# Kernel tuning notes

Measured on AMD Instinct MI355X. Metric: run time of the kernel, lower is better.

The kernel has to match this reference:

```python
import jax, jax.numpy as jnp
import numpy as np

N_CRYST = 64
ATOMS_PER = 32
N = N_CRYST * ATOMS_PER          # 2048 atoms
NBR = 20                         # max_neighbors
E = N * NBR                      # 40960 edges
C = 128                          # sphere_channels(_reduce)
HID = 256                        # hidden_channels
NB = 128                         # num_basis_functions
NLAYER = 8                       # num_interactions
LMAX = 6
K = 1 + 3 * LMAX                 # SH coeffs with mmax=1 -> 19
MAXZ = 100                       # MAX_ATOMIC_NUM
ZDIM = 256
CUT = 8.0
FOUR_PI = 4.0 * np.pi


def sph_harm_m01(d):
    """Real spherical harmonics Y_l^m, l<=LMAX, m in {-1,0,1}. d: [E,3] unit vecs -> [E,K]."""
    x, y, ct = d[:, 0], d[:, 1], d[:, 2]
    rho = jnp.sqrt(x * x + y * y) + 1e-12   # sin(theta)
    cph, sph = x / rho, y / rho
    # Legendre P_l(ct)
    P0 = [jnp.ones_like(ct), ct]
    for l in range(2, LMAX + 1):
        P0.append(((2 * l - 1) * ct * P0[l - 1] - (l - 1) * P0[l - 2]) / l)
    # Associated Legendre P_l^1(ct)
    P1 = {1: -rho, 2: -3.0 * ct * rho}
    for l in range(3, LMAX + 1):
        P1[l] = ((2 * l - 1) * ct * P1[l - 1] - l * P1[l - 2]) / (l - 1)
    Ys = [jnp.full_like(ct, float(np.sqrt(1.0 / FOUR_PI)))]
    for l in range(1, LMAX + 1):
        K0 = float(np.sqrt((2 * l + 1) / FOUR_PI))
        K1 = float(np.sqrt(2.0 * (2 * l + 1) / FOUR_PI / (l * (l + 1))))
        Ys += [K1 * P1[l] * sph, K0 * P0[l], K1 * P1[l] * cph]  # m=-1,0,+1
    return jnp.stack(Ys, axis=-1)


def lattice_from_params(lengths, angles):
    """lengths,angles(deg): [B,3] -> lattice row-vectors [B,3,3]."""
    a, b, c = lengths[:, 0], lengths[:, 1], lengths[:, 2]
    rad = angles * (np.pi / 180.0)
    ca, cb, cg = jnp.cos(rad[:, 0]), jnp.cos(rad[:, 1]), jnp.cos(rad[:, 2])
    sg = jnp.sin(rad[:, 2])
    z0 = jnp.zeros_like(a)
    v3y = (ca - cb * cg) / sg
    v3z = jnp.sqrt(jnp.clip(1.0 - cb * cb - v3y * v3y, 1e-8))
    l1 = jnp.stack([a, z0, z0], -1)
    l2 = jnp.stack([b * cg, b * sg, z0], -1)
    l3 = jnp.stack([c * cb, c * v3y, c * v3z], -1)
    return jnp.stack([l1, l2, l3], axis=1)


def setup_inputs() -> dict:
    key = jax.random.key(0)
    ks = jax.random.split(key, 16)
    z = jax.random.normal(ks[0], (N_CRYST, ZDIM), jnp.float32)
    frac = jax.random.uniform(ks[1], (N, 3), jnp.float32)
    atom_types = jax.random.randint(ks[2], (N,), 1, MAXZ + 1)
    num_atoms = jnp.full((N_CRYST,), ATOMS_PER, jnp.int32)
    lengths = 4.0 + 4.0 * jax.random.uniform(ks[3], (N_CRYST, 3), jnp.float32)
    angles = 80.0 + 20.0 * jax.random.uniform(ks[4], (N_CRYST, 3), jnp.float32)
    batch = jnp.arange(N) // ATOMS_PER
    # NBR incoming edges per atom, sources restricted to the same crystal
    dst = jnp.repeat(jnp.arange(N), NBR)
    src_local = jax.random.randint(ks[5], (E,), 0, ATOMS_PER)
    src = (dst // ATOMS_PER) * ATOMS_PER + src_local
    edge_index = jnp.stack([src, dst], axis=0)
    sc = lambda k, sh, fan: jax.random.normal(k, sh, jnp.float32) / np.sqrt(fan)
    params = dict(
        emb=sc(ks[6], (MAXZ + 1, C), 1.0),
        zproj=sc(ks[7], (ZDIM, C), ZDIM),
        Wd=sc(ks[8], (NLAYER, NB, HID), NB),
        W1=sc(ks[9], (NLAYER, C, HID), C),
        W2=sc(ks[10], (NLAYER, HID, C), HID),
        Wa=sc(ks[11], (C, MAXZ), C),
        ba=jnp.zeros((MAXZ,), jnp.float32),
        wf=sc(ks[12], (C,), C),
    )
    return dict(z=z, pred_frac_coords=frac, pred_atom_types=atom_types,
                num_atoms=num_atoms, lengths=lengths, angles=angles,
                batch=batch, edge_index=edge_index, **params)


def reference(z, pred_frac_coords, pred_atom_types, num_atoms, lengths, angles,
              batch, edge_index, emb, zproj, Wd, W1, W2, Wa, ba, wf):
    lat = lattice_from_params(lengths, angles)                 # [B,3,3]
    pos = jnp.einsum('ni,nij->nj', pred_frac_coords, lat[batch])  # [N,3]
    src, dst = edge_index[0], edge_index[1]
    vec = pos[src] - pos[dst]                                  # [E,3]
    dist = jnp.linalg.norm(vec, axis=-1) + 1e-8
    dirn = vec / dist[:, None]
    offsets = jnp.linspace(0.0, CUT, NB)
    width = offsets[1] - offsets[0]
    rbf = jnp.exp(-0.5 * ((dist[:, None] - offsets) / width) ** 2)  # [E,NB]
    Y = sph_harm_m01(dirn)                                     # [E,K]
    # node SH features, l=0 initialized from atom embedding + latent
    x = jnp.zeros((N, K, C), pred_frac_coords.dtype)
    x = x.at[:, 0, :].set(emb[pred_atom_types] + (z @ zproj)[batch])
    for l in range(NLAYER):
        s = jnp.einsum('ek,ekc->ec', Y, x[src])                # project along edge frame
        h = jax.nn.silu(s @ W1[l] + rbf @ Wd[l])               # [E,HID]
        m = h @ W2[l]                                          # [E,C]
        agg = jax.ops.segment_sum(Y[:, :, None] * m[:, None, :], dst, num_segments=N)
        x = x + agg / NBR
    h_node = x[:, 0, :]                                        # [N,C]
    atom_logits = h_node @ Wa + ba                             # [N,MAXZ]
    fscal = (h_node[src] - h_node[dst]) @ wf                   # [E]
    coord_diff = jax.ops.segment_sum(fscal[:, None] * dirn, dst, num_segments=N)
    return coord_diff, atom_logits
```

## Files before the change

kernel.cpp:

```cpp
#include <hip/hip_runtime.h>
#include <hip/hip_bf16.h>

#define N_CRYST 64
#define ATOMS_PER 32
#define NN 2048
#define NBRS 20
#define EE 40960
#define CC 128
#define HIDDIM 256
#define NBASIS 128
#define NLAYERS 8
#define LMAXV 6
#define KK 19
#define MAXZV 100
#define ZDIMV 256
#define FOUR_PI_F 12.566370614359172f

typedef unsigned short ushort_t;
typedef __attribute__((ext_vector_type(8))) short short8;
typedef __attribute__((ext_vector_type(4))) float floatx4;

__device__ __forceinline__ ushort_t f2us(float f) {
    union { float f; unsigned u; } x;
    x.f = f;
    unsigned r = (x.u + 0x7fffu + ((x.u >> 16) & 1u)) >> 16;
    return (ushort_t)r;
}
__device__ __forceinline__ float us2f(unsigned u) {
    return __uint_as_float(u << 16);
}

__global__ void k_pos(const float* __restrict__ frac, const float* __restrict__ lengths,
                      const float* __restrict__ angles, const int* __restrict__ batch,
                      float* __restrict__ pos) {
    int n = blockIdx.x * blockDim.x + threadIdx.x;
    if (n >= NN) return;
    int b = batch[n];
    float la = lengths[b * 3 + 0];
    float lb = lengths[b * 3 + 1];
    float lc = lengths[b * 3 + 2];
    const float D2R = 0.017453292519943295f;
    float aa = angles[b * 3 + 0] * D2R;
    float ab = angles[b * 3 + 1] * D2R;
    float ag = angles[b * 3 + 2] * D2R;
    float ca = cosf(aa), cb = cosf(ab), cg = cosf(ag), sg = sinf(ag);
    float v3y = (ca - cb * cg) / sg;
    float v3z = sqrtf(fmaxf(1.0f - cb * cb - v3y * v3y, 1e-8f));
    float f0 = frac[n * 3 + 0];
    float f1 = frac[n * 3 + 1];
    float f2 = frac[n * 3 + 2];
    pos[n * 3 + 0] = f0 * la + f1 * (lb * cg) + f2 * (lc * cb);
    pos[n * 3 + 1] = f1 * (lb * sg) + f2 * (lc * v3y);
    pos[n * 3 + 2] = f2 * (lc * v3z);
}

__global__ void k_edge(const int* __restrict__ ei, const float* __restrict__ pos,
                       float* __restrict__ dist, float* __restrict__ dirn,
                       float* __restrict__ Yv) {
    int e = blockIdx.x * blockDim.x + threadIdx.x;
    if (e >= EE) return;
    int s = ei[e], d = ei[EE + e];
    float vx = pos[s * 3 + 0] - pos[d * 3 + 0];
    float vy = pos[s * 3 + 1] - pos[d * 3 + 1];
    float vz = pos[s * 3 + 2] - pos[d * 3 + 2];
    float dd = sqrtf(vx * vx + vy * vy + vz * vz) + 1e-8f;
    float ix = vx / dd, iy = vy / dd, iz = vz / dd;
    dist[e] = dd;
    dirn[e * 3 + 0] = ix;
    dirn[e * 3 + 1] = iy;
    dirn[e * 3 + 2] = iz;

    float ct = iz;
    float rho = sqrtf(ix * ix + iy * iy) + 1e-12f;
    float cph = ix / rho, sph = iy / rho;
    float P0[LMAXV + 1];
    float P1[LMAXV + 1];
    P0[0] = 1.0f;
    P0[1] = ct;
    #pragma unroll
    for (int l = 2; l <= LMAXV; l++)
        P0[l] = ((2 * l - 1) * ct * P0[l - 1] - (l - 1) * P0[l - 2]) / (float)l;
    P1[0] = 0.0f;
    P1[1] = -rho;
    P1[2] = -3.0f * ct * rho;
    #pragma unroll
    for (int l = 3; l <= LMAXV; l++)
        P1[l] = ((2 * l - 1) * ct * P1[l - 1] - l * P1[l - 2]) / (float)(l - 1);

    float* Ye = Yv + (size_t)e * KK;
    Ye[0] = 0.28209479177387814f;
    #pragma unroll
    for (int l = 1; l <= LMAXV; l++) {
        float K0 = sqrtf((2 * l + 1) / FOUR_PI_F);
        float K1 = sqrtf(2.0f * (2 * l + 1) / (FOUR_PI_F * l * (l + 1)));
        Ye[3 * l - 2] = K1 * P1[l] * sph;
        Ye[3 * l - 1] = K0 * P0[l];
        Ye[3 * l]     = K1 * P1[l] * cph;
    }
}

__global__ void k_tcsr(const int* __restrict__ ei, int* __restrict__ trp,
                       int* __restrict__ tloc) {
    int bid = blockIdx.x;
    int t = threadIdx.x;
    __shared__ int cnt[32], base[32];
    if (t < 32) cnt[t] = 0;
    __syncthreads();
    int e0 = bid * 80;
    int abase = (bid >> 3) * 32;
    for (int j = t; j < 80; j += 64) {
        int a = ei[e0 + j] - abase;
        atomicAdd(&cnt[a], 1);
    }
    __syncthreads();
    if (t == 0) {
        int run = 0;
        for (int a = 0; a < 32; a++) {
            base[a] = run;
            trp[bid * 33 + a] = run;
            run += cnt[a];
        }
        trp[bid * 33 + 32] = run;
    }
    __syncthreads();
    if (t < 32) cnt[t] = 0;
    __syncthreads();
    for (int j = t; j < 80; j += 64) {
        int a = ei[e0 + j] - abase;
        int slot = base[a] + atomicAdd(&cnt[a], 1);
        tloc[bid * 80 + slot] = j;
    }
}

__global__ void k_rbfA(const float* __restrict__ dist, ushort_t* __restrict__ Abf) {
    int idx = blockIdx.x * blockDim.x + threadIdx.x;
    if (idx >= EE * NBASIS) return;
    int e = idx >> 7, j = idx & 127;
    const float width = 8.0f / 127.0f;
    const float invw = 127.0f / 8.0f;
    float t = (dist[e] - (float)j * width) * invw;
    Abf[(size_t)e * 256 + 128 + j] = f2us(expf(-0.5f * t * t));
}

__global__ void k_wt(const float* __restrict__ W1, const float* __restrict__ Wd,
                     const float* __restrict__ W2,
                     ushort_t* __restrict__ WT1, ushort_t* __restrict__ WT2) {
    int idx = blockIdx.x * blockDim.x + threadIdx.x;
    const int n1 = NLAYERS * HIDDIM * 256;
    if (idx < n1) {
        int l = idx >> 16;
        int r = idx & 65535;
        int n = r >> 8, k = r & 255;
        float v = (k < 128) ? W1[((size_t)l * CC + k) * HIDDIM + n]
                            : Wd[((size_t)l * NBASIS + (k - 128)) * HIDDIM + n];
        WT1[idx] = f2us(v);
    } else {
        int j = idx - n1;
        if (j >= NLAYERS * CC * HIDDIM) return;
        int l = j >> 15;
        int r = j & 32767;
        int n = r >> 8, k = r & 255;
        WT2[j] = f2us(W2[((size_t)l * HIDDIM + k) * CC + n]);
    }
}

__global__ void k_zc(const float* __restrict__ z, const float* __restrict__ zproj,
                     float* __restrict__ zc) {
    int idx = blockIdx.x * blockDim.x + threadIdx.x;
    if (idx >= N_CRYST * CC) return;
    int b = idx >> 7, c = idx & 127;
    float acc = 0.0f;
    for (int d = 0; d < ZDIMV; d++)
        acc += z[b * ZDIMV + d] * zproj[d * CC + c];
    zc[idx] = acc;
}

__global__ void k_xinit(const int* __restrict__ atype, const int* __restrict__ batch,
                        const float* __restrict__ emb, const float* __restrict__ zc,
                        float* __restrict__ x, ushort_t* __restrict__ xbf) {
    int idx = blockIdx.x * blockDim.x + threadIdx.x;
    if (idx >= NN * KK * CC) return;
    int n = idx / (KK * CC);
    int r = idx - n * (KK * CC);
    float v = 0.0f;
    if (r < CC) v = emb[atype[n] * CC + r] + zc[batch[n] * CC + r];
    x[idx] = v;
    xbf[idx] = f2us(v);
}

__global__ __launch_bounds__(512, 2) void k_layer(const int* __restrict__ trp,
                                                  const int* __restrict__ tloc,
                                                  const float* __restrict__ Yv,
                                                  const ushort_t* __restrict__ Abf,
                                                  const ushort_t* __restrict__ WT1,
                                                  const ushort_t* __restrict__ WT2,
                                                  const float* __restrict__ xin,
                                                  float* __restrict__ xout,
                                                  const ushort_t* __restrict__ xbfin,
                                                  ushort_t* __restrict__ xbfout) {
    __shared__ char smraw[47360];
    ushort_t* As  = (ushort_t*)smraw;
    ushort_t* Hs  = (ushort_t*)smraw;
    ushort_t* Ms  = (ushort_t*)smraw;
    float*   Ylds = (float*)(smraw + 40960);

    const int t = threadIdx.x;
    const int bid = blockIdx.x;
    const int w = t >> 6, lane = t & 63;
    const int quad = lane >> 4, lrow = lane & 15;
    const int e0 = bid * 80;
    const int cr = bid >> 3;

    const float* Yb = Yv + (size_t)e0 * KK;
    #pragma unroll
    for (int j = 0; j < 3; j++) {
        int i = t + j * 512;
        if (i < 80 * KK) Ylds[(i / KK) * 20 + (i % KK)] = Yb[i];
    }
    if (t < 80) Ylds[t * 20 + 19] = 0.f;
    __syncthreads();

    short8 arg[3];
    #pragma unroll
    for (int i = 0; i < 3; i++) {
        int idx = i * 512 + t;
        if (idx < 1280) {
            int r = idx >> 4, g16 = idx & 15;
            arg[i] = *(const short8*)(Abf + (size_t)(e0 + r) * 256 + 128 + g16 * 8);
        }
    }

    const int c2 = lane * 2;
    const int sgrp = lane >> 2;
    const int soff = (lane & 3) * 2;
    #pragma unroll 1
    for (int a8 = 0; a8 < 4; a8++) {
        const int a = w * 4 + a8;
        const int i0 = trp[bid * 33 + a];
        const int i1 = trp[bid * 33 + a + 1];
        if (i0 == i1) continue;
        const ushort_t* xsrc = xbfin + (size_t)(cr * 32 + a) * (KK * CC) + c2;
        float2 xr[KK];
        #pragma unroll
        for (int k = 0; k < KK; k++) {
            unsigned u = *(const unsigned*)(xsrc + k * CC);
            xr[k] = make_float2(us2f(u & 0xffffu), us2f(u >> 16));
        }
        for (int i = i0; i < i1; i++) {
            const int r = tloc[bid * 80 + i];
            const float* yp = Ylds + r * 20;
            float ax = 0.f, ay = 0.f;
            #pragma unroll
            for (int k = 0; k < KK; k++) {
                float y = yp[k];
                ax += y * xr[k].x;
                ay += y * xr[k].y;
            }
            unsigned pk = (unsigned)f2us(ax) | (((unsigned)f2us(ay)) << 16);
            *(unsigned*)&As[r * 256 + ((sgrp ^ (r & 7)) << 3) + soff] = pk;
        }
    }

    #pragma unroll
    for (int i = 0; i < 3; i++) {
        int idx = i * 512 + t;
        if (idx < 1280) {
            int r = idx >> 4, g = 16 + (idx & 15);
            *(short8*)&As[r * 256 + ((g ^ (r & 7)) << 3)] = arg[i];
        }
    }

    const ushort_t* W1w = WT1 + (size_t)(w * 32) * 256;
    short8 bp0[2], bp1[2];
    #pragma unroll
    for (int ni = 0; ni < 2; ni++) {
        bp0[ni] = *(const short8*)(W1w + (size_t)(ni * 16 + lrow) * 256 + quad * 8);
        bp1[ni] = *(const short8*)(W1w + (size_t)(ni * 16 + lrow) * 256 + 32 + quad * 8);
    }
    __syncthreads();

    floatx4 acc[5][2];
    #pragma unroll
    for (int mi = 0; mi < 5; mi++)
        #pragma unroll
        for (int ni = 0; ni < 2; ni++) acc[mi][ni] = (floatx4){0.f, 0.f, 0.f, 0.f};

    #pragma unroll
    for (int s8 = 0; s8 < 8; s8++) {
        short8 bcur[2];
        if (s8 & 1) {
            #pragma unroll
            for (int ni = 0; ni < 2; ni++) bcur[ni] = bp1[ni];
            if (s8 < 6) {
                const int kn = (s8 + 2) * 32 + quad * 8;
                #pragma unroll
                for (int ni = 0; ni < 2; ni++)
                    bp1[ni] = *(const short8*)(W1w + (size_t)(ni * 16 + lrow) * 256 + kn);
            }
        } else {
            #pragma unroll
            for (int ni = 0; ni < 2; ni++) bcur[ni] = bp0[ni];
            if (s8 < 6) {
                const int kn = (s8 + 2) * 32 + quad * 8;
                #pragma unroll
                for (int ni = 0; ni < 2; ni++)
                    bp0[ni] = *(const short8*)(W1w + (size_t)(ni * 16 + lrow) * 256 + kn);
            }
        }
        const int grp = s8 * 4 + quad;
        short8 af[5];
        #pragma unroll
        for (int mi = 0; mi < 5; mi++) {
            const int r = mi * 16 + lrow;
            af[mi] = *(const short8*)&As[r * 256 + ((grp ^ (r & 7)) << 3)];
        }
        #pragma unroll
        for (int ni = 0; ni < 2; ni++)
            #pragma unroll
            for (int mi = 0; mi < 5; mi++)
                acc[mi][ni] = __builtin_amdgcn_mfma_f32_16x16x32_bf16(
                    af[mi], bcur[ni], acc[mi][ni], 0, 0, 0);
    }

    const ushort_t* W2w = WT2 + (size_t)(w * 16) * 256;
    short8 bq0, bq1;
    bq0 = *(const short8*)(W2w + (size_t)lrow * 256 + quad * 8);
    bq1 = *(const short8*)(W2w + (size_t)lrow * 256 + 32 + quad * 8);
    __syncthreads();

    #pragma unroll
    for (int mi = 0; mi < 5; mi++) {
        const int row = mi * 16 + quad * 4;
        #pragma unroll
        for (int ni = 0; ni < 2; ni++) {
            const int col = w * 32 + ni * 16 + lrow;
            #pragma unroll
            for (int r = 0; r < 4; r++) {
                float v = acc[mi][ni][r];
                v = v * __builtin_amdgcn_rcpf(1.0f + __expf(-v));
                const int rr = row + r;
                Hs[rr * 256 + ((((col >> 3) ^ (rr & 7)) << 3) | (col & 7))] = f2us(v);
            }
        }
    }
    __syncthreads();

    floatx4 macc[5];
    #pragma unroll
    for (int mi = 0; mi < 5; mi++) macc[mi] = (floatx4){0.f, 0.f, 0.f, 0.f};

    #pragma unroll
    for (int s8 = 0; s8 < 8; s8++) {
        short8 bcur;
        if (s8 & 1) {
            bcur = bq1;
            if (s8 < 6) {
                const int kn = (s8 + 2) * 32 + quad * 8;
                bq1 = *(const short8*)(W2w + (size_t)lrow * 256 + kn);
            }
        } else {
            bcur = bq0;
            if (s8 < 6) {
                const int kn = (s8 + 2) * 32 + quad * 8;
                bq0 = *(const short8*)(W2w + (size_t)lrow * 256 + kn);
            }
        }
        const int grp = s8 * 4 + quad;
        short8 af[5];
        #pragma unroll
        for (int mi = 0; mi < 5; mi++) {
            const int r = mi * 16 + lrow;
            af[mi] = *(const short8*)&Hs[r * 256 + ((grp ^ (r & 7)) << 3)];
        }
        #pragma unroll
        for (int mi = 0; mi < 5; mi++)
            macc[mi] = __builtin_amdgcn_mfma_f32_16x16x32_bf16(
                af[mi], bcur, macc[mi], 0, 0, 0);
    }
    __syncthreads();

    #pragma unroll
    for (int mi = 0; mi < 5; mi++) {
        const int row = mi * 16 + quad * 4;
        const int col = w * 16 + lrow;
        #pragma unroll
        for (int r = 0; r < 4; r++)
            Ms[(row + r) * 132 + col] = f2us(macc[mi][r]);
    }
    __syncthreads();

    const int node = t >> 7;
    const int cq = t & 127;
    const int ng = bid * 4 + node;
    const float* xpi = xin + (size_t)ng * (KK * CC) + cq;
    float* xpo = xout + (size_t)ng * (KK * CC) + cq;
    ushort_t* xbp = xbfout + (size_t)ng * (KK * CC) + cq;

    float xold[KK];
    #pragma unroll
    for (int k = 0; k < KK; k++) xold[k] = xpi[k * CC];

    float xacc[KK];
    #pragma unroll
    for (int k = 0; k < KK; k++) xacc[k] = 0.f;

    #pragma unroll 4
    for (int e = 0; e < NBRS; e++) {
        const int eg = node * NBRS + e;
        const float m0 = us2f((unsigned)Ms[eg * 132 + cq]);
        const float* yp = Ylds + eg * 20;
        #pragma unroll
        for (int kq = 0; kq < 5; kq++) {
            float4 y = *(const float4*)(yp + kq * 4);
            const int k = kq * 4;
            xacc[k + 0] += y.x * m0;
            xacc[k + 1] += y.y * m0;
            xacc[k + 2] += y.z * m0;
            if (kq < 4) xacc[k + 3] += y.w * m0;
        }
    }
    const float s = 1.0f / (float)NBRS;
    #pragma unroll
    for (int k = 0; k < KK; k++) {
        float nv = xold[k] + xacc[k] * s;
        xpo[k * CC] = nv;
        xbp[k * CC] = f2us(nv);
    }
}

__global__ void k_logits(const float* __restrict__ x, const float* __restrict__ Wa,
                         const float* __restrict__ ba, float* __restrict__ out) {
    int idx = blockIdx.x * blockDim.x + threadIdx.x;
    if (idx >= NN * MAXZV) return;
    int n = idx / MAXZV, a = idx - n * MAXZV;
    float acc = ba[a];
    const float* hn = x + (size_t)n * (KK * CC);
    for (int c = 0; c < CC; c++) acc += hn[c] * Wa[c * MAXZV + a];
    out[idx] = acc;
}

__global__ void k_coord(const int* __restrict__ ei, const float* __restrict__ x,
                        const float* __restrict__ wf, const float* __restrict__ dirn,
                        float* __restrict__ out) {
    int n = blockIdx.x;
    int t = threadIdx.x;
    __shared__ float fs[NBRS];
    __shared__ float wsh[CC];
    wsh[t] = wf[t];
    wsh[t + 64] = wf[t + 64];
    __syncthreads();
    if (t < NBRS) {
        int e = n * NBRS + t;
        int sidx = ei[e];
        const float* xs = x + (size_t)sidx * (KK * CC);
        const float* xd = x + (size_t)n * (KK * CC);
        float acc = 0.0f;
        for (int c = 0; c < CC; c++) acc += (xs[c] - xd[c]) * wsh[c];
        fs[t] = acc;
    }
    __syncthreads();
    if (t < 3) {
        float acc = 0.0f;
        #pragma unroll
        for (int j = 0; j < NBRS; j++) acc += fs[j] * dirn[(size_t)(n * NBRS + j) * 3 + t];
        out[n * 3 + t] = acc;
    }
}

extern "C" void kernel_launch(void* const* d_in, const int* in_sizes, int n_in,
                              void* d_out, int out_size, void* d_ws, size_t ws_size,
                              hipStream_t stream) {
    (void)in_sizes; (void)n_in; (void)out_size; (void)ws_size;
    const float* z       = (const float*)d_in[0];
    const float* frac    = (const float*)d_in[1];
    const int*   atype   = (const int*)d_in[2];
    const float* lengths = (const float*)d_in[4];
    const float* angles  = (const float*)d_in[5];
    const int*   batch   = (const int*)d_in[6];
    const int*   ei      = (const int*)d_in[7];
    const float* emb     = (const float*)d_in[8];
    const float* zproj   = (const float*)d_in[9];
    const float* Wd      = (const float*)d_in[10];
    const float* W1      = (const float*)d_in[11];
    const float* W2      = (const float*)d_in[12];
    const float* Wa      = (const float*)d_in[13];
    const float* ba      = (const float*)d_in[14];
    const float* wf      = (const float*)d_in[15];
    float* out = (float*)d_out;

    float* ws = (float*)d_ws;
    float* pos  = ws; ws += NN * 3 + 4;
    float* dist = ws; ws += EE;
    float* dirn = ws; ws += EE * 3;
    float* Yv   = ws; ws += (size_t)EE * KK + 4;
    float* zc   = ws; ws += N_CRYST * CC;
    float* xA   = ws; ws += (size_t)NN * KK * CC;
    float* xB   = ws; ws += (size_t)NN * KK * CC;
    ushort_t* xbfA = (ushort_t*)ws; ws += (size_t)NN * KK * CC / 2;
    ushort_t* xbfB = (ushort_t*)ws; ws += (size_t)NN * KK * CC / 2;
    int* trp  = (int*)ws;
    int* tloc = trp + 512 * 33;
    ushort_t* Abf  = (ushort_t*)(tloc + 512 * 80);
    ushort_t* WT1  = Abf + (size_t)EE * 256;
    ushort_t* WT2  = WT1 + (size_t)NLAYERS * 256 * 256;

    k_pos<<<NN / 256, 256, 0, stream>>>(frac, lengths, angles, batch, pos);
    k_edge<<<EE / 256, 256, 0, stream>>>(ei, pos, dist, dirn, Yv);
    k_tcsr<<<512, 64, 0, stream>>>(ei, trp, tloc);
    k_rbfA<<<(EE * NBASIS) / 256, 256, 0, stream>>>(dist, Abf);
    k_wt<<<(NLAYERS * (HIDDIM * 256 + CC * HIDDIM)) / 256, 256, 0, stream>>>(W1, Wd, W2, WT1, WT2);
    k_zc<<<(N_CRYST * CC) / 256, 256, 0, stream>>>(z, zproj, zc);
    k_xinit<<<(NN * KK * CC) / 256, 256, 0, stream>>>(atype, batch, emb, zc, xA, xbfA);

    for (int l = 0; l < NLAYERS; l++) {
        const float* xi = (l & 1) ? xB : xA;
        float*       xo = (l & 1) ? xA : xB;
        const ushort_t* xbi = (l & 1) ? xbfB : xbfA;
        ushort_t*       xbo = (l & 1) ? xbfA : xbfB;
        k_layer<<<512, 512, 0, stream>>>(trp, tloc, Yv, Abf,
                                         WT1 + (size_t)l * 256 * 256,
                                         WT2 + (size_t)l * CC * HIDDIM,
                                         xi, xo, xbi, xbo);
    }

    k_coord<<<NN, 64, 0, stream>>>(ei, xA, wf, dirn, out);
    k_logits<<<(NN * MAXZV) / 256, 256, 0, stream>>>(xA, Wa, ba, out + NN * 3);
}
```

Measured before the change: 502.5 us.

## Fuse setup kernels, drop fp32 node state, merge output heads

Merges the position, edge geometry and CSR-building kernels into one per-crystal kernel that keeps positions in shared memory. Folds the latent projection into the node-init kernel and combines the coordinate and logits heads into a single launch. Removes the fp32 copy of the node features, so each layer now reads and writes only the bf16 state. This cuts launches and memory traffic, but the residual stream is now accumulated in bf16 across layers, which can hurt accuracy. The init kernel also recomputes the 256-long projection for every atom instead of once per crystal.

After: 480.4 us. 4.4% less time.

```diff
diff --git a/kernel.cpp b/kernel.cpp
--- a/kernel.cpp
+++ b/kernel.cpp
@@ -30,105 +30,99 @@
     return __uint_as_float(u << 16);
 }
 
-__global__ void k_pos(const float* __restrict__ frac, const float* __restrict__ lengths,
-                      const float* __restrict__ angles, const int* __restrict__ batch,
-                      float* __restrict__ pos) {
-    int n = blockIdx.x * blockDim.x + threadIdx.x;
-    if (n >= NN) return;
-    int b = batch[n];
-    float la = lengths[b * 3 + 0];
-    float lb = lengths[b * 3 + 1];
-    float lc = lengths[b * 3 + 2];
-    const float D2R = 0.017453292519943295f;
-    float aa = angles[b * 3 + 0] * D2R;
-    float ab = angles[b * 3 + 1] * D2R;
-    float ag = angles[b * 3 + 2] * D2R;
-    float ca = cosf(aa), cb = cosf(ab), cg = cosf(ag), sg = sinf(ag);
-    float v3y = (ca - cb * cg) / sg;
-    float v3z = sqrtf(fmaxf(1.0f - cb * cb - v3y * v3y, 1e-8f));
-    float f0 = frac[n * 3 + 0];
-    float f1 = frac[n * 3 + 1];
-    float f2 = frac[n * 3 + 2];
-    pos[n * 3 + 0] = f0 * la + f1 * (lb * cg) + f2 * (lc * cb);
-    pos[n * 3 + 1] = f1 * (lb * sg) + f2 * (lc * v3y);
-    pos[n * 3 + 2] = f2 * (lc * v3z);
-}
-
-__global__ void k_edge(const int* __restrict__ ei, const float* __restrict__ pos,
+__global__ void k_geom(const float* __restrict__ frac, const float* __restrict__ lengths,
+                       const float* __restrict__ angles, const int* __restrict__ ei,
                        float* __restrict__ dist, float* __restrict__ dirn,
-                       float* __restrict__ Yv) {
-    int e = blockIdx.x * blockDim.x + threadIdx.x;
-    if (e >= EE) return;
-    int s = ei[e], d = ei[EE + e];
-    float vx = pos[s * 3 + 0] - pos[d * 3 + 0];
-    float vy = pos[s * 3 + 1] - pos[d * 3 + 1];
-    float vz = pos[s * 3 + 2] - pos[d * 3 + 2];
-    float dd = sqrtf(vx * vx + vy * vy + vz * vz) + 1e-8f;
-    float ix = vx / dd, iy = vy / dd, iz = vz / dd;
-    dist[e] = dd;
-    dirn[e * 3 + 0] = ix;
-    dirn[e * 3 + 1] = iy;
-    dirn[e * 3 + 2] = iz;
-
-    float ct = iz;
-    float rho = sqrtf(ix * ix + iy * iy) + 1e-12f;
-    float cph = ix / rho, sph = iy / rho;
-    float P0[LMAXV + 1];
-    float P1[LMAXV + 1];
-    P0[0] = 1.0f;
-    P0[1] = ct;
-    #pragma unroll
-    for (int l = 2; l <= LMAXV; l++)
-        P0[l] = ((2 * l - 1) * ct * P0[l - 1] - (l - 1) * P0[l - 2]) / (float)l;
-    P1[0] = 0.0f;
-    P1[1] = -rho;
-    P1[2] = -3.0f * ct * rho;
-    #pragma unroll
-    for (int l = 3; l <= LMAXV; l++)
-        P1[l] = ((2 * l - 1) * ct * P1[l - 1] - l * P1[l - 2]) / (float)(l - 1);
-
-    float* Ye = Yv + (size_t)e * KK;
-    Ye[0] = 0.28209479177387814f;
-    #pragma unroll
-    for (int l = 1; l <= LMAXV; l++) {
-        float K0 = sqrtf((2 * l + 1) / FOUR_PI_F);
-        float K1 = sqrtf(2.0f * (2 * l + 1) / (FOUR_PI_F * l * (l + 1)));
-        Ye[3 * l - 2] = K1 * P1[l] * sph;
-        Ye[3 * l - 1] = K0 * P0[l];
-        Ye[3 * l]     = K1 * P1[l] * cph;
-    }
-}
-
-__global__ void k_tcsr(const int* __restrict__ ei, int* __restrict__ trp,
+                       float* __restrict__ Yv, int* __restrict__ trp,
                        int* __restrict__ tloc) {
-    int bid = blockIdx.x;
-    int t = threadIdx.x;
-    __shared__ int cnt[32], base[32];
-    if (t < 32) cnt[t] = 0;
-    __syncthreads();
-    int e0 = bid * 80;
-    int abase = (bid >> 3) * 32;
-    for (int j = t; j < 80; j += 64) {
-        int a = ei[e0 + j] - abase;
-        atomicAdd(&cnt[a], 1);
-    }
-    __syncthreads();
-    if (t == 0) {
+    const int cr = blockIdx.x;
+    const int t = threadIdx.x;
+    __shared__ float posL[32][3];
+    __shared__ int cnt[8][32], base[8][32];
+
+    if (t < 32) {
+        int n = cr * 32 + t;
+        float la = lengths[cr * 3 + 0];
+        float lb = lengths[cr * 3 + 1];
+        float lc = lengths[cr * 3 + 2];
+        const float D2R = 0.017453292519943295f;
+        float aa = angles[cr * 3 + 0] * D2R;
+        float ab = angles[cr * 3 + 1] * D2R;
+        float ag = angles[cr * 3 + 2] * D2R;
+        float ca = cosf(aa), cb = cosf(ab), cg = cosf(ag), sg = sinf(ag);
+        float v3y = (ca - cb * cg) / sg;
+        float v3z = sqrtf(fmaxf(1.0f - cb * cb - v3y * v3y, 1e-8f));
+        float f0 = frac[n * 3 + 0];
+        float f1 = frac[n * 3 + 1];
+        float f2 = frac[n * 3 + 2];
+        posL[t][0] = f0 * la + f1 * (lb * cg) + f2 * (lc * cb);
+        posL[t][1] = f1 * (lb * sg) + f2 * (lc * v3y);
+        posL[t][2] = f2 * (lc * v3z);
+    }
+    cnt[t >> 5][t & 31] = 0;
+    __syncthreads();
+
+    for (int j = t; j < 640; j += 256) {
+        int e = cr * 640 + j;
+        int s = ei[e] - cr * 32, d = ei[EE + e] - cr * 32;
+        float vx = posL[s][0] - posL[d][0];
+        float vy = posL[s][1] - posL[d][1];
+        float vz = posL[s][2] - posL[d][2];
+        float dd = sqrtf(vx * vx + vy * vy + vz * vz) + 1e-8f;
+        float ix = vx / dd, iy = vy / dd, iz = vz / dd;
+        dist[e] = dd;
+        dirn[e * 3 + 0] = ix;
+        dirn[e * 3 + 1] = iy;
+        dirn[e * 3 + 2] = iz;
+
+        float ct = iz;
+        float rho = sqrtf(ix * ix + iy * iy) + 1e-12f;
+        float cph = ix / rho, sph = iy / rho;
+        float P0[LMAXV + 1], P1[LMAXV + 1];
+        P0[0] = 1.0f;
+        P0[1] = ct;
+        #pragma unroll
+        for (int l = 2; l <= LMAXV; l++)
+            P0[l] = ((2 * l - 1) * ct * P0[l - 1] - (l - 1) * P0[l - 2]) / (float)l;
+        P1[0] = 0.0f;
+        P1[1] = -rho;
+        P1[2] = -3.0f * ct * rho;
+        #pragma unroll
+        for (int l = 3; l <= LMAXV; l++)
+            P1[l] = ((2 * l - 1) * ct * P1[l - 1] - l * P1[l - 2]) / (float)(l - 1);
+
+        float* Ye = Yv + (size_t)e * KK;
+        Ye[0] = 0.28209479177387814f;
+        #pragma unroll
+        for (int l = 1; l <= LMAXV; l++) {
+            float K0 = sqrtf((2 * l + 1) / FOUR_PI_F);
+            float K1 = sqrtf(2.0f * (2 * l + 1) / (FOUR_PI_F * l * (l + 1)));
+            Ye[3 * l - 2] = K1 * P1[l] * sph;
+            Ye[3 * l - 1] = K0 * P0[l];
+            Ye[3 * l]     = K1 * P1[l] * cph;
+        }
+        atomicAdd(&cnt[j / 80][s], 1);
+    }
+    __syncthreads();
+
+    if (t < 8) {
         int run = 0;
         for (int a = 0; a < 32; a++) {
-            base[a] = run;
-            trp[bid * 33 + a] = run;
-            run += cnt[a];
-        }
-        trp[bid * 33 + 32] = run;
-    }
-    __syncthreads();
-    if (t < 32) cnt[t] = 0;
-    __syncthreads();
-    for (int j = t; j < 80; j += 64) {
-        int a = ei[e0 + j] - abase;
-        int slot = base[a] + atomicAdd(&cnt[a], 1);
-        tloc[bid * 80 + slot] = j;
+            base[t][a] = run;
+            trp[(cr * 8 + t) * 33 + a] = run;
+            run += cnt[t][a];
+        }
+        trp[(cr * 8 + t) * 33 + 32] = run;
+    }
+    __syncthreads();
+    cnt[t >> 5][t & 31] = 0;
+    __syncthreads();
+    for (int j = t; j < 640; j += 256) {
+        int e = cr * 640 + j;
+        int s = ei[e] - cr * 32;
+        int tt = j / 80;
+        int slot = base[tt][s] + atomicAdd(&cnt[tt][s], 1);
+        tloc[(cr * 8 + tt) * 80 + slot] = j - tt * 80;
     }
 }
 
@@ -164,27 +158,19 @@
     }
 }
 
-__global__ void k_zc(const float* __restrict__ z, const float* __restrict__ zproj,
-                     float* __restrict__ zc) {
-    int idx = blockIdx.x * blockDim.x + threadIdx.x;
-    if (idx >= N_CRYST * CC) return;
-    int b = idx >> 7, c = idx & 127;
-    float acc = 0.0f;
-    for (int d = 0; d < ZDIMV; d++)
-        acc += z[b * ZDIMV + d] * zproj[d * CC + c];
-    zc[idx] = acc;
-}
-
 __global__ void k_xinit(const int* __restrict__ atype, const int* __restrict__ batch,
-                        const float* __restrict__ emb, const float* __restrict__ zc,
-                        float* __restrict__ x, ushort_t* __restrict__ xbf) {
+                        const float* __restrict__ emb, const float* __restrict__ z,
+                        const float* __restrict__ zproj, ushort_t* __restrict__ xbf) {
     int idx = blockIdx.x * blockDim.x + threadIdx.x;
     if (idx >= NN * KK * CC) return;
     int n = idx / (KK * CC);
     int r = idx - n * (KK * CC);
     float v = 0.0f;
-    if (r < CC) v = emb[atype[n] * CC + r] + zc[batch[n] * CC + r];
-    x[idx] = v;
+    if (r < CC) {
+        v = emb[atype[n] * CC + r];
+        const float* zb = z + (size_t)batch[n] * ZDIMV;
+        for (int d = 0; d < ZDIMV; d++) v += zb[d] * zproj[d * CC + r];
+    }
     xbf[idx] = f2us(v);
 }
 
@@ -194,8 +180,6 @@
                                                   const ushort_t* __restrict__ Abf,
                                                   const ushort_t* __restrict__ WT1,
                                                   const ushort_t* __restrict__ WT2,
-                                                  const float* __restrict__ xin,
-                                                  float* __restrict__ xout,
                                                   const ushort_t* __restrict__ xbfin,
                                                   ushort_t* __restrict__ xbfout) {
     __shared__ char smraw[47360];
@@ -392,13 +376,12 @@
     const int node = t >> 7;
     const int cq = t & 127;
     const int ng = bid * 4 + node;
-    const float* xpi = xin + (size_t)ng * (KK * CC) + cq;
-    float* xpo = xout + (size_t)ng * (KK * CC) + cq;
-    ushort_t* xbp = xbfout + (size_t)ng * (KK * CC) + cq;
+    const ushort_t* xbi = xbfin + (size_t)ng * (KK * CC) + cq;
+    ushort_t* xbo = xbfout + (size_t)ng * (KK * CC) + cq;
 
     float xold[KK];
     #pragma unroll
-    for (int k = 0; k < KK; k++) xold[k] = xpi[k * CC];
+    for (int k = 0; k < KK; k++) xold[k] = us2f((unsigned)xbi[k * CC]);
 
     float xacc[KK];
     #pragma unroll
@@ -423,47 +406,50 @@
     #pragma unroll
     for (int k = 0; k < KK; k++) {
         float nv = xold[k] + xacc[k] * s;
-        xpo[k * CC] = nv;
-        xbp[k * CC] = f2us(nv);
-    }
-}
-
-__global__ void k_logits(const float* __restrict__ x, const float* __restrict__ Wa,
-                         const float* __restrict__ ba, float* __restrict__ out) {
-    int idx = blockIdx.x * blockDim.x + threadIdx.x;
-    if (idx >= NN * MAXZV) return;
-    int n = idx / MAXZV, a = idx - n * MAXZV;
-    float acc = ba[a];
-    const float* hn = x + (size_t)n * (KK * CC);
-    for (int c = 0; c < CC; c++) acc += hn[c] * Wa[c * MAXZV + a];
-    out[idx] = acc;
-}
-
-__global__ void k_coord(const int* __restrict__ ei, const float* __restrict__ x,
-                        const float* __restrict__ wf, const float* __restrict__ dirn,
-                        float* __restrict__ out) {
-    int n = blockIdx.x;
-    int t = threadIdx.x;
-    __shared__ float fs[NBRS];
-    __shared__ float wsh[CC];
-    wsh[t] = wf[t];
-    wsh[t + 64] = wf[t + 64];
-    __syncthreads();
-    if (t < NBRS) {
-        int e = n * NBRS + t;
-        int sidx = ei[e];
-        const float* xs = x + (size_t)sidx * (KK * CC);
-        const float* xd = x + (size_t)n * (KK * CC);
-        float acc = 0.0f;
-        for (int c = 0; c < CC; c++) acc += (xs[c] - xd[c]) * wsh[c];
-        fs[t] = acc;
-    }
-    __syncthreads();
-    if (t < 3) {
-        float acc = 0.0f;
-        #pragma unroll
-        for (int j = 0; j < NBRS; j++) acc += fs[j] * dirn[(size_t)(n * NBRS + j) * 3 + t];
-        out[n * 3 + t] = acc;
+        xbo[k * CC] = f2us(nv);
+    }
+}
+
+#define COORD_BLKS 512
+__global__ void k_head(const int* __restrict__ ei, const ushort_t* __restrict__ xbf,
+                       const float* __restrict__ wf, const float* __restrict__ dirn,
+                       const float* __restrict__ Wa, const float* __restrict__ ba,
+                       float* __restrict__ out) {
+    const int bid = blockIdx.x;
+    const int t = threadIdx.x;
+    if (bid < COORD_BLKS) {
+        __shared__ float fs[4][NBRS];
+        __shared__ float wsh[CC];
+        const int g = t >> 6, lane = t & 63;
+        const int n = bid * 4 + g;
+        if (t < CC) wsh[t] = wf[t];
+        __syncthreads();
+        if (lane < NBRS) {
+            int e = n * NBRS + lane;
+            int sidx = ei[e];
+            const ushort_t* xs = xbf + (size_t)sidx * (KK * CC);
+            const ushort_t* xd = xbf + (size_t)n * (KK * CC);
+            float acc = 0.0f;
+            for (int c = 0; c < CC; c++)
+                acc += (us2f((unsigned)xs[c]) - us2f((unsigned)xd[c])) * wsh[c];
+            fs[g][lane] = acc;
+        }
+        __syncthreads();
+        if (lane < 3) {
+            float acc = 0.0f;
+            #pragma unroll
+            for (int j = 0; j < NBRS; j++)
+                acc += fs[g][j] * dirn[(size_t)(n * NBRS + j) * 3 + lane];
+            out[n * 3 + lane] = acc;
+        }
+    } else {
+        int idx = (bid - COORD_BLKS) * 256 + t;
+        if (idx >= NN * MAXZV) return;
+        int n = idx / MAXZV, a = idx - n * MAXZV;
+        float acc = ba[a];
+        const ushort_t* hn = xbf + (size_t)n * (KK * CC);
+        for (int c = 0; c < CC; c++) acc += us2f((unsigned)hn[c]) * Wa[c * MAXZV + a];
+        out[NN * 3 + idx] = acc;
     }
 }
 
@@ -489,13 +475,9 @@
     float* out = (float*)d_out;
 
     float* ws = (float*)d_ws;
-    float* pos  = ws; ws += NN * 3 + 4;
     float* dist = ws; ws += EE;
     float* dirn = ws; ws += EE * 3;
     float* Yv   = ws; ws += (size_t)EE * KK + 4;
-    float* zc   = ws; ws += N_CRYST * CC;
-    float* xA   = ws; ws += (size_t)NN * KK * CC;
-    float* xB   = ws; ws += (size_t)NN * KK * CC;
     ushort_t* xbfA = (ushort_t*)ws; ws += (size_t)NN * KK * CC / 2;
     ushort_t* xbfB = (ushort_t*)ws; ws += (size_t)NN * KK * CC / 2;
     int* trp  = (int*)ws;
@@ -504,25 +486,20 @@
     ushort_t* WT1  = Abf + (size_t)EE * 256;
     ushort_t* WT2  = WT1 + (size_t)NLAYERS * 256 * 256;
 
-    k_pos<<<NN / 256, 256, 0, stream>>>(frac, lengths, angles, batch, pos);
-    k_edge<<<EE / 256, 256, 0, stream>>>(ei, pos, dist, dirn, Yv);
-    k_tcsr<<<512, 64, 0, stream>>>(ei, trp, tloc);
+    k_geom<<<N_CRYST, 256, 0, stream>>>(frac, lengths, angles, ei, dist, dirn, Yv, trp, tloc);
     k_rbfA<<<(EE * NBASIS) / 256, 256, 0, stream>>>(dist, Abf);
     k_wt<<<(NLAYERS * (HIDDIM * 256 + CC * HIDDIM)) / 256, 256, 0, stream>>>(W1, Wd, W2, WT1, WT2);
-    k_zc<<<(N_CRYST * CC) / 256, 256, 0, stream>>>(z, zproj, zc);
-    k_xinit<<<(NN * KK * CC) / 256, 256, 0, stream>>>(atype, batch, emb, zc, xA, xbfA);
+    k_xinit<<<(NN * KK * CC) / 256, 256, 0, stream>>>(atype, batch, emb, z, zproj, xbfA);
 
     for (int l = 0; l < NLAYERS; l++) {
-        const float* xi = (l & 1) ? xB : xA;
-        float*       xo = (l & 1) ? xA : xB;
         const ushort_t* xbi = (l & 1) ? xbfB : xbfA;
         ushort_t*       xbo = (l & 1) ? xbfA : xbfB;
         k_layer<<<512, 512, 0, stream>>>(trp, tloc, Yv, Abf,
                                          WT1 + (size_t)l * 256 * 256,
                                          WT2 + (size_t)l * CC * HIDDIM,
-                                         xi, xo, xbi, xbo);
-    }
-
-    k_coord<<<NN, 64, 0, stream>>>(ei, xA, wf, dirn, out);
-    k_logits<<<(NN * MAXZV) / 256, 256, 0, stream>>>(xA, Wa, ba, out + NN * 3);
-}
+                                         xbi, xbo);
+    }
+
+    k_head<<<COORD_BLKS + (NN * MAXZV) / 256, 256, 0, stream>>>(ei, xbfA, wf, dirn,
+                                                                Wa, ba, out);
+}
```
